# Kernel tuning notes

Hardware: AMD Instinct MI355X
Metric: run time of the kernel (lower is better)

Reference implementation:

```python
import jax, jax.numpy as jnp
import numpy as np
import math

E = 1024   # embed_size
H = 16     # heads arg (actual per-'head' dim due to source's reshape quirk)
G = E // H # 64 head-groups (treated as heads in the source code)
FF = 4 * E


def setup_inputs() -> dict:
    key = jax.random.key(0)
    ks = jax.random.split(key, 12)
    s = 1.0 / math.sqrt(E)
    inp = {
        'x': jax.random.normal(ks[0], (2, 1024, E), dtype=jnp.float32),
        # linear weights stored as (in, out); torch Linear computes x @ W.T + b
        'Wq': jax.random.uniform(ks[1], (E, E), jnp.float32, -s, s),
        'Wk': jax.random.uniform(ks[2], (E, E), jnp.float32, -s, s),
        'Wv': jax.random.uniform(ks[3], (E, E), jnp.float32, -s, s),
        'Wo': jax.random.uniform(ks[4], (E, E), jnp.float32, -s, s),
        'bo': jax.random.uniform(ks[5], (E,), jnp.float32, -s, s),
        'W1': jax.random.uniform(ks[6], (E, FF), jnp.float32, -s, s),
        'b1': jax.random.uniform(ks[7], (FF,), jnp.float32, -s, s),
        'W2': jax.random.uniform(ks[8], (FF, E), jnp.float32, -1.0 / math.sqrt(FF), 1.0 / math.sqrt(FF)),
        'b2': jax.random.uniform(ks[9], (E,), jnp.float32, -s, s),
        'g1': jnp.ones((E,), jnp.float32), 'be1': jnp.zeros((E,), jnp.float32),
        'g2': jnp.ones((E,), jnp.float32), 'be2': jnp.zeros((E,), jnp.float32),
    }
    return inp


def _layernorm(x, g, b, eps=1e-5):
    mu = jnp.mean(x, axis=-1, keepdims=True)
    var = jnp.mean(jnp.square(x - mu), axis=-1, keepdims=True)
    return (x - mu) * jax.lax.rsqrt(var + eps) * g + b


def reference(x, Wq, Wk, Wv, Wo, bo, W1, b1, W2, b2, g1, be1, g2, be2):
    B, S, _ = x.shape
    # QKV projections; faithful to source: split E into (G=E//H groups, H dims),
    # group axis acts as the 'head' axis, per-head dim is H, scale = sqrt(H).
    def split(t):  # [B,S,E] -> [B,G,S,H]
        return t.reshape(B, S, G, H).transpose(0, 2, 1, 3)
    q = split(x @ Wq)
    k = split(x @ Wk)
    v = split(x @ Wv)
    att = jnp.einsum('bgsh,bgth->bgst', q, k) / math.sqrt(H)
    causal = jnp.tril(jnp.ones((S, S), dtype=bool))  # mask==1 above diag -> -inf
    att = jnp.where(causal, att, -jnp.inf)
    att = jax.nn.softmax(att, axis=-1)
    y = jnp.einsum('bgst,bgth->bgsh', att, v)          # [B,G,S,H]
    y = y.transpose(0, 2, 1, 3).reshape(B, S, E)
    attn_out = y @ Wo + bo
    # dropout is identity at inference
    x = _layernorm(attn_out + x, g1, be1)
    ff = jax.nn.relu(x @ W1 + b1) @ W2 + b2
    x = _layernorm(ff + x, g2, be2)
    return x
```

## Files before the change

### kernel.cpp

```cpp
#include <hip/hip_runtime.h>
#include <hip/hip_bf16.h>
#include <math.h>


#define E_DIM 1024
#define S_LEN 1024
#define B_SZ  2
#define G_HEADS 64
#define H_DIM 16
#define FF_DIM 4096
#define M_ROWS (B_SZ * S_LEN)
#define QKV_N  (3 * E_DIM)

#define QSCALE 0.36067376022224085f

using bf16x8 = __attribute__((ext_vector_type(8))) short;
using f32x4  = __attribute__((ext_vector_type(4))) float;
using f32x16 = __attribute__((ext_vector_type(16))) float;
using ushort8 = __attribute__((ext_vector_type(8))) unsigned short;

static __device__ __forceinline__ unsigned short f2bf(float f) {
    union { float f; unsigned int u; } x; x.f = f;
    unsigned int r = x.u + 0x7fff + ((x.u >> 16) & 1);
    return (unsigned short)(r >> 16);
}
static __device__ __forceinline__ unsigned int pack2(float a, float b) {
    union { __hip_bfloat162 h; unsigned int u; } c;
    c.h = __float22bfloat162_rn(float2{a, b});
    return c.u;
}

__global__ __launch_bounds__(256) void cast_kernel(
    const float* __restrict__ X, unsigned short* __restrict__ Xb)
{
    const size_t i = ((size_t)blockIdx.x * 256 + threadIdx.x) * 8;
    float4 a = *(const float4*)(X + i);
    float4 b = *(const float4*)(X + i + 4);
    ushort8 o;
    o[0] = f2bf(a.x); o[1] = f2bf(a.y); o[2] = f2bf(a.z); o[3] = f2bf(a.w);
    o[4] = f2bf(b.x); o[5] = f2bf(b.y); o[6] = f2bf(b.z); o[7] = f2bf(b.w);
    *(ushort8*)(Xb + i) = o;
}

__global__ __launch_bounds__(256) void transpose_cast4_kernel(
    const float* __restrict__ W0, const float* __restrict__ W1_,
    const float* __restrict__ W2_, const float* __restrict__ W3_,
    unsigned short* __restrict__ Wt012, unsigned short* __restrict__ Wt3)
{
    __shared__ float tile[32][33];
    const int z = blockIdx.z;
    const float* W = (z == 0) ? W0 : (z == 1) ? W1_ : (z == 2) ? W2_ : W3_;
    unsigned short* Wo = (z < 3) ? (Wt012 + (size_t)z * E_DIM * E_DIM) : Wt3;
    const int n0 = blockIdx.x * 32, k0 = blockIdx.y * 32;
    const int t = threadIdx.x;
    const int r = t >> 3;
    const int c = (t & 7) * 4;

    float4 v = *(const float4*)(W + (size_t)(k0 + r) * E_DIM + n0 + c);
    tile[r][c] = v.x; tile[r][c + 1] = v.y; tile[r][c + 2] = v.z; tile[r][c + 3] = v.w;
    __syncthreads();

    ushort4 o;
    o.x = f2bf(tile[c + 0][r]); o.y = f2bf(tile[c + 1][r]);
    o.z = f2bf(tile[c + 2][r]); o.w = f2bf(tile[c + 3][r]);
    *(ushort4*)(Wo + (size_t)(n0 + r) * E_DIM + k0 + c) = o;
}

__global__ __launch_bounds__(256) void transpose_cast_ff_kernel(
    const float* __restrict__ W1_, const float* __restrict__ W2_,
    unsigned short* __restrict__ W1t, unsigned short* __restrict__ W2t)
{
    __shared__ float tile[32][33];
    const int z = blockIdx.z;
    const float* W = z ? W2_ : W1_;
    unsigned short* Wt = z ? W2t : W1t;
    const int N = z ? E_DIM : FF_DIM;
    const int K = z ? FF_DIM : E_DIM;
    const int n0 = (z ? blockIdx.y : blockIdx.x) * 32;
    const int k0 = (z ? blockIdx.x : blockIdx.y) * 32;
    const int t = threadIdx.x;
    const int r = t >> 3;
    const int c = (t & 7) * 4;

    float4 v = *(const float4*)(W + (size_t)(k0 + r) * N + n0 + c);
    tile[r][c] = v.x; tile[r][c + 1] = v.y; tile[r][c + 2] = v.z; tile[r][c + 3] = v.w;
    __syncthreads();

    ushort4 o;
    o.x = f2bf(tile[c + 0][r]); o.y = f2bf(tile[c + 1][r]);
    o.z = f2bf(tile[c + 2][r]); o.w = f2bf(tile[c + 3][r]);
    *(ushort4*)(Wt + (size_t)(n0 + r) * K + k0 + c) = o;
}

template<int ACT, int OUTBF, int SCALEQ>
__global__ __launch_bounds__(256) void gemm_mfma(
    const unsigned short* __restrict__ A,
    const unsigned short* __restrict__ Bt,
    const float* __restrict__ bias,
    float* __restrict__ C0, float* __restrict__ C1,
    unsigned short* __restrict__ Cb,
    int Krow, int Kchunk, int ldc)
{
    __shared__ __align__(16) unsigned short lds[2][12288];

    const int tid  = threadIdx.x;
    const int wave = tid >> 6;
    const int lane = tid & 63;
    const int wr = wave >> 1;
    const int wc = wave & 1;
    const int row0 = blockIdx.y * 128;
    const int col0 = blockIdx.x * 64;
    const int kbase = blockIdx.z * Kchunk;

    const int lr = lane & 15;
    const int lk = (lane >> 4) * 8;

    const int srow = (lane >> 2);
    const int scol = (lane & 3) * 8;

    f32x4 acc[4][2] = {};

    auto STAGE1 = [&](unsigned short* dstA, unsigned short* dstB, int k0) {
        #pragma unroll
        for (int i = 0; i < 2; ++i) {
            const int ci = wave + i * 4;
            const unsigned short* src =
                A + (size_t)(row0 + ci * 16 + srow) * Krow + k0 + scol;
            __builtin_amdgcn_global_load_lds(
                (const __attribute__((address_space(1))) void*)src,
                (__attribute__((address_space(3))) void*)(dstA + ci * 512),
                16, 0, 0);
        }
        {
            const unsigned short* src =
                Bt + (size_t)(col0 + wave * 16 + srow) * Krow + k0 + scol;
            __builtin_amdgcn_global_load_lds(
                (const __attribute__((address_space(1))) void*)src,
                (__attribute__((address_space(3))) void*)(dstB + wave * 512),
                16, 0, 0);
        }
    };
    auto STAGE = [&](int buf, int k0) {
        STAGE1(&lds[buf][0],    &lds[buf][4096],  k0);
        STAGE1(&lds[buf][6144], &lds[buf][10240], k0 + 32);
    };
    auto COMPUTE = [&](int buf, int sub) {
        const unsigned short* As = &lds[buf][sub * 6144];
        const unsigned short* Bs = As + 4096;
        bf16x8 a[4], b[2];
        #pragma unroll
        for (int mi = 0; mi < 4; ++mi)
            a[mi] = *(const bf16x8*)(As + (wr * 64 + mi * 16 + lr) * 32 + lk);
        #pragma unroll
        for (int ni = 0; ni < 2; ++ni)
            b[ni] = *(const bf16x8*)(Bs + (wc * 32 + ni * 16 + lr) * 32 + lk);
        #pragma unroll
        for (int mi = 0; mi < 4; ++mi)
            #pragma unroll
            for (int ni = 0; ni < 2; ++ni)
                acc[mi][ni] = __builtin_amdgcn_mfma_f32_16x16x32_bf16(
                    a[mi], b[ni], acc[mi][ni], 0, 0, 0);
    };

    const int nt = Kchunk >> 6;

    STAGE(0, kbase);
    asm volatile("s_waitcnt vmcnt(0)" ::: "memory");
    __builtin_amdgcn_s_barrier();

    int cur = 0;
    for (int t = 0; t < nt; ++t) {
        if (t + 1 < nt) STAGE(cur ^ 1, kbase + (t + 1) * 64);
        COMPUTE(cur, 0);
        COMPUTE(cur, 1);
        asm volatile("s_waitcnt vmcnt(0)" ::: "memory");
        __builtin_amdgcn_s_barrier();
        cur ^= 1;
    }

    float* Cw = blockIdx.z ? C1 : C0;
    #pragma unroll
    for (int mi = 0; mi < 4; ++mi) {
        #pragma unroll
        for (int ni = 0; ni < 2; ++ni) {
            const int cc  = col0 + wc * 32 + ni * 16 + (lane & 15);
            const int rr0 = row0 + wr * 64 + mi * 16 + ((lane >> 4) << 2);
            const float bv = bias ? bias[cc] : 0.f;
            #pragma unroll
            for (int j = 0; j < 4; ++j) {
                float v = acc[mi][ni][j] + bv;
                if (ACT == 1) v = fmaxf(v, 0.f);
                if (SCALEQ && cc < E_DIM) v *= QSCALE;
                if (OUTBF) Cb[(size_t)(rr0 + j) * ldc + cc] = f2bf(v);
                else       Cw[(size_t)(rr0 + j) * ldc + cc] = v;
            }
        }
    }
}

__global__ __launch_bounds__(256) void attn_kernel(
    const unsigned short* __restrict__ qkv, unsigned short* __restrict__ Yb)
{
    __shared__ __align__(16) unsigned short Ks[2][64 * 16];
    __shared__ __align__(16) unsigned short Vs[2][64 * 16];

    const int bi = blockIdx.x >> 7;
    const int bg = blockIdx.x & 127;
    const int g  = bg & (G_HEADS - 1);
    const int b  = bg >> 6;
    const int tid  = threadIdx.x;
    const int lane = tid & 63;
    const int l31  = lane & 31;
    const int hi   = lane >> 5;
    const int wv   = tid >> 6;
    const int tokb = b * S_LEN;

    const int cblk = 28 - 4 * bi;
    const int q0   = (cblk + wv) * 32;
    const int qrow = q0 + l31;
    const int nt64 = (cblk + 4) >> 1;

    const bf16x8 qf = *(const bf16x8*)(
        qkv + (size_t)(tokb + qrow) * QKV_N + g * H_DIM + hi * 8);

    f32x16 acc = {};
    const f32x16 fz = {};

    const int kv  = tid >> 7;
    const int h64 = (tid >> 6) & 1;
    const int skey  = h64 * 32 + (lane >> 1);
    const int shalf = lane & 1;
    const size_t sgo = (size_t)(g * H_DIM + (1 + kv) * E_DIM + shalf * 8);
    unsigned short* const sdst = (kv ? &Vs[0][0] : &Ks[0][0]) + h64 * 512;

    auto STAGE = [&](int buf, int t64) {
        const unsigned short* src =
            qkv + (size_t)(tokb + t64 * 64 + skey) * QKV_N + sgo;
        __builtin_amdgcn_global_load_lds(
            (const __attribute__((address_space(1))) void*)src,
            (__attribute__((address_space(3))) void*)(sdst + buf * 1024),
            16, 0, 0);
    };

    auto PROCESS = [&](int cur, int sub, int t0) {
        const bf16x8 kf = *(const bf16x8*)(&Ks[cur][(sub * 32 + l31) * 16 + hi * 8]);
        __builtin_amdgcn_s_setprio(1);
        f32x16 s = __builtin_amdgcn_mfma_f32_32x32x16_bf16(kf, qf, fz, 0, 0, 0);
        __builtin_amdgcn_s_setprio(0);

        float pq[16];
        if (t0 == q0) {
            #pragma unroll
            for (int r = 0; r < 16; ++r) {
                const int key = t0 + (r & 3) + 8 * (r >> 2) + 4 * hi;
                pq[r] = (key > qrow) ? 0.f : exp2f(s[r]);
            }
        } else {
            #pragma unroll
            for (int r = 0; r < 16; ++r) pq[r] = exp2f(s[r]);
        }

        unsigned int cw[8], ow[8];
        #pragma unroll
        for (int r2 = 0; r2 < 8; ++r2) cw[r2] = pack2(pq[2 * r2], pq[2 * r2 + 1]);
        #pragma unroll
        for (int r2 = 0; r2 < 8; ++r2)
            ow[r2] = (unsigned int)__shfl_xor((int)cw[r2], 32);

        const bool lo = (hi == 0);
        union { uint4 u; bf16x8 v; } pf0, pf1;
        pf0.u.x = lo ? cw[0] : ow[2];
        pf0.u.y = lo ? cw[1] : ow[3];
        pf0.u.z = lo ? ow[0] : cw[2];
        pf0.u.w = lo ? ow[1] : cw[3];
        pf1.u.x = lo ? cw[4] : ow[6];
        pf1.u.y = lo ? cw[5] : ow[7];
        pf1.u.z = lo ? ow[4] : cw[6];
        pf1.u.w = lo ? ow[5] : cw[7];

        const int hcol = l31 & 15;
        const bool isl = (l31 == 16);
        union { unsigned short s2[8]; bf16x8 v; } vb0, vb1;
        #pragma unroll
        for (int e = 0; e < 8; ++e) {
            const int kr = sub * 32 + hi * 8 + e;
            vb0.s2[e] = isl ? (unsigned short)0x3F80 : Vs[cur][kr * 16 + hcol];
            vb1.s2[e] = isl ? (unsigned short)0x3F80 : Vs[cur][(kr + 16) * 16 + hcol];
        }
        __builtin_amdgcn_s_setprio(1);
        acc = __builtin_amdgcn_mfma_f32_32x32x16_bf16(pf0.v, vb0.v, acc, 0, 0, 0);
        acc = __builtin_amdgcn_mfma_f32_32x32x16_bf16(pf1.v, vb1.v, acc, 0, 0, 0);
        __builtin_amdgcn_s_setprio(0);
    };

    STAGE(0, 0);
    asm volatile("s_waitcnt vmcnt(0)" ::: "memory");
    __builtin_amdgcn_s_barrier();

    int cur = 0;
    for (int t = 0; t < nt64; ++t) {
        if (t + 1 < nt64) STAGE(cur ^ 1, t + 1);
        #pragma unroll
        for (int sub = 0; sub < 2; ++sub) {
            const int t0 = t * 64 + sub * 32;
            if (t0 <= q0) PROCESS(cur, sub, t0);
        }
        asm volatile("s_waitcnt vmcnt(0)" ::: "memory");
        __builtin_amdgcn_s_barrier();
        cur ^= 1;
    }

    float linv[16];
    #pragma unroll
    for (int r = 0; r < 16; ++r) {
        const float lr_ = __shfl(acc[r], (hi << 5) + 16);
        linv[r] = __builtin_amdgcn_rcpf(lr_);
    }
    if (l31 < H_DIM) {
        #pragma unroll
        for (int r = 0; r < 16; ++r) {
            const int q = (r & 3) + 8 * (r >> 2) + 4 * hi;
            Yb[(size_t)(tokb + q0 + q) * E_DIM + g * H_DIM + l31] =
                f2bf(acc[r] * linv[r]);
        }
    }
}

__global__ __launch_bounds__(256) void add_ln2_kernel(
    const float* __restrict__ P0, const float* __restrict__ P1,
    const float* __restrict__ bias, const float* __restrict__ resid,
    const float* __restrict__ g, const float* __restrict__ be,
    float* __restrict__ O, unsigned short* __restrict__ Ob)
{
    const int row = blockIdx.x;
    const size_t base = (size_t)row * E_DIM;
    const int tid = threadIdx.x;

    float v[4];
    float s = 0.f;
    #pragma unroll
    for (int i = 0; i < 4; ++i) {
        int c = tid + i * 256;
        v[i] = P0[base + c] + P1[base + c] + bias[c] + resid[base + c];
        s += v[i];
    }

    __shared__ float red[256];
    red[tid] = s; __syncthreads();
    for (int st = 128; st >= 1; st >>= 1) {
        if (tid < st) red[tid] += red[tid + st];
        __syncthreads();
    }
    const float mu = red[0] * (1.f / E_DIM);
    __syncthreads();

    float s2 = 0.f;
    #pragma unroll
    for (int i = 0; i < 4; ++i) { float d = v[i] - mu; s2 += d * d; }
    red[tid] = s2; __syncthreads();
    for (int st = 128; st >= 1; st >>= 1) {
        if (tid < st) red[tid] += red[tid + st];
        __syncthreads();
    }
    const float rs = rsqrtf(red[0] * (1.f / E_DIM) + 1e-5f);

    #pragma unroll
    for (int i = 0; i < 4; ++i) {
        int c = tid + i * 256;
        float o = (v[i] - mu) * rs * g[c] + be[c];
        O[base + c] = o;
        if (Ob) Ob[base + c] = f2bf(o);
    }
}

extern "C" void kernel_launch(void* const* d_in, const int* in_sizes, int n_in,
                              void* d_out, int out_size, void* d_ws, size_t ws_size,
                              hipStream_t stream)
{
    const float* x  = (const float*)d_in[0];
    const float* Wq = (const float*)d_in[1];
    const float* Wk = (const float*)d_in[2];
    const float* Wv = (const float*)d_in[3];
    const float* Wo = (const float*)d_in[4];
    const float* bo = (const float*)d_in[5];
    const float* W1 = (const float*)d_in[6];
    const float* b1 = (const float*)d_in[7];
    const float* W2 = (const float*)d_in[8];
    const float* b2 = (const float*)d_in[9];
    const float* g1  = (const float*)d_in[10];
    const float* be1 = (const float*)d_in[11];
    const float* g2  = (const float*)d_in[12];
    const float* be2 = (const float*)d_in[13];

    char* W = (char*)d_ws;
    const size_t MB = 1024 * 1024;
    unsigned short* xb   = (unsigned short*)(W + 0 * MB);
    unsigned short* Wqkt = (unsigned short*)(W + 4 * MB);
    unsigned short* qkvb = (unsigned short*)(W + 10 * MB);
    unsigned short* yb   = (unsigned short*)(W + 22 * MB);
    unsigned short* Wot  = (unsigned short*)(W + 26 * MB);
    float* P_o0          = (float*)(W + 4 * MB);
    float* P_o1          = (float*)(W + 12 * MB);
    unsigned short* x1b  = (unsigned short*)(W + 20 * MB);
    float* x1            = (float*)(W + 28 * MB);
    unsigned short* W1t  = (unsigned short*)(W + 36 * MB);
    unsigned short* W2t  = (unsigned short*)(W + 44 * MB);
    unsigned short* ff1b = (unsigned short*)(W + 0 * MB);
    float* P_f1          = (float*)(W + 16 * MB);
    float* out           = (float*)d_out;

    dim3 blk(256);

    cast_kernel<<<dim3((M_ROWS * E_DIM) / (256 * 8)), blk, 0, stream>>>(x, xb);
    transpose_cast4_kernel<<<dim3(32, 32, 4), blk, 0, stream>>>(Wq, Wk, Wv, Wo, Wqkt, Wot);
    transpose_cast_ff_kernel<<<dim3(128, 32, 2), blk, 0, stream>>>(W1, W2, W1t, W2t);
    gemm_mfma<0, 1, 1><<<dim3(QKV_N / 64, M_ROWS / 128, 1), blk, 0, stream>>>(
        xb, Wqkt, nullptr, nullptr, nullptr, qkvb, E_DIM, E_DIM, QKV_N);
    attn_kernel<<<dim3(B_SZ * G_HEADS * 8), blk, 0, stream>>>(qkvb, yb);
    gemm_mfma<0, 0, 0><<<dim3(E_DIM / 64, M_ROWS / 128, 2), blk, 0, stream>>>(
        yb, Wot, nullptr, P_o0, P_o1, nullptr, E_DIM, E_DIM / 2, E_DIM);
    add_ln2_kernel<<<dim3(M_ROWS), blk, 0, stream>>>(P_o0, P_o1, bo, x, g1, be1, x1, x1b);
    gemm_mfma<1, 1, 0><<<dim3(FF_DIM / 64, M_ROWS / 128, 1), blk, 0, stream>>>(
        x1b, W1t, b1, nullptr, nullptr, ff1b, E_DIM, E_DIM, FF_DIM);
    gemm_mfma<0, 0, 0><<<dim3(E_DIM / 64, M_ROWS / 128, 2), blk, 0, stream>>>(
        ff1b, W2t, nullptr, out, P_f1, nullptr, FF_DIM, FF_DIM / 2, E_DIM);
    add_ln2_kernel<<<dim3(M_ROWS), blk, 0, stream>>>(out, P_f1, b2, x1, g2, be2, out, nullptr);
}
```

Measured before the change: 170.6 us.

## Stage V transposed in LDS and use permlane32 swap for P fragments

V tiles are now loaded into registers and written transposed (with a padded stride and a constant ones row for the softmax denominator) into LDS, so each lane fetches its B operand with two 16-byte vector reads instead of sixteen scalar LDS reads with per-element selects. The cross-half exchange of the P fragment uses v_permlane32_swap instead of eight shfl_xor plus selects. This trades the asynchronous global-to-LDS copy for V for a register load plus scattered scalar LDS stores per tile, and adds an lgkmcnt wait before the barrier.

```diff
diff --git a/kernel.cpp b/kernel.cpp
--- a/kernel.cpp
+++ b/kernel.cpp
@@ -13,6 +13,9 @@
 #define QKV_N  (3 * E_DIM)
 
 #define QSCALE 0.36067376022224085f
+
+#define VT_STRIDE 72
+#define VT_BUF    1224
 
 using bf16x8 = __attribute__((ext_vector_type(8))) short;
 using f32x4  = __attribute__((ext_vector_type(4))) float;
@@ -201,8 +204,8 @@
 __global__ __launch_bounds__(256) void attn_kernel(
     const unsigned short* __restrict__ qkv, unsigned short* __restrict__ Yb)
 {
-    __shared__ __align__(16) unsigned short Ks[2][64 * 16];
-    __shared__ __align__(16) unsigned short Vs[2][64 * 16];
+    __shared__ __align__(16) unsigned short Ks[2][1024];
+    __shared__ __align__(16) unsigned short Vt[2][VT_BUF];
 
     const int bi = blockIdx.x >> 7;
     const int bg = blockIdx.x & 127;
@@ -231,16 +234,28 @@
     const int skey  = h64 * 32 + (lane >> 1);
     const int shalf = lane & 1;
     const size_t sgo = (size_t)(g * H_DIM + (1 + kv) * E_DIM + shalf * 8);
-    unsigned short* const sdst = (kv ? &Vs[0][0] : &Ks[0][0]) + h64 * 512;
-
-    auto STAGE = [&](int buf, int t64) {
+
+    auto STAGE = [&](int buf, int t64, ushort8& vreg) {
         const unsigned short* src =
             qkv + (size_t)(tokb + t64 * 64 + skey) * QKV_N + sgo;
-        __builtin_amdgcn_global_load_lds(
-            (const __attribute__((address_space(1))) void*)src,
-            (__attribute__((address_space(3))) void*)(sdst + buf * 1024),
-            16, 0, 0);
-    };
+        if (kv == 0) {
+            __builtin_amdgcn_global_load_lds(
+                (const __attribute__((address_space(1))) void*)src,
+                (__attribute__((address_space(3))) void*)(&Ks[buf][h64 * 512]),
+                16, 0, 0);
+        } else {
+            vreg = *(const ushort8*)src;
+        }
+    };
+    auto WRITE_V = [&](int buf, const ushort8& vreg) {
+        if (kv == 1) {
+            #pragma unroll
+            for (int j = 0; j < 8; ++j)
+                Vt[buf][(shalf * 8 + j) * VT_STRIDE + skey] = vreg[j];
+        }
+    };
+
+    const int vrow = (l31 == 16) ? 16 : (l31 & 15);
 
     auto PROCESS = [&](int cur, int sub, int t0) {
         const bf16x8 kf = *(const bf16x8*)(&Ks[cur][(sub * 32 + l31) * 16 + hi * 8]);
@@ -260,52 +275,64 @@
             for (int r = 0; r < 16; ++r) pq[r] = exp2f(s[r]);
         }
 
-        unsigned int cw[8], ow[8];
+        unsigned int cw[8];
         #pragma unroll
         for (int r2 = 0; r2 < 8; ++r2) cw[r2] = pack2(pq[2 * r2], pq[2 * r2 + 1]);
-        #pragma unroll
-        for (int r2 = 0; r2 < 8; ++r2)
-            ow[r2] = (unsigned int)__shfl_xor((int)cw[r2], 32);
-
-        const bool lo = (hi == 0);
+
         union { uint4 u; bf16x8 v; } pf0, pf1;
-        pf0.u.x = lo ? cw[0] : ow[2];
-        pf0.u.y = lo ? cw[1] : ow[3];
-        pf0.u.z = lo ? ow[0] : cw[2];
-        pf0.u.w = lo ? ow[1] : cw[3];
-        pf1.u.x = lo ? cw[4] : ow[6];
-        pf1.u.y = lo ? cw[5] : ow[7];
-        pf1.u.z = lo ? ow[4] : cw[6];
-        pf1.u.w = lo ? ow[5] : cw[7];
-
-        const int hcol = l31 & 15;
-        const bool isl = (l31 == 16);
-        union { unsigned short s2[8]; bf16x8 v; } vb0, vb1;
-        #pragma unroll
-        for (int e = 0; e < 8; ++e) {
-            const int kr = sub * 32 + hi * 8 + e;
-            vb0.s2[e] = isl ? (unsigned short)0x3F80 : Vs[cur][kr * 16 + hcol];
-            vb1.s2[e] = isl ? (unsigned short)0x3F80 : Vs[cur][(kr + 16) * 16 + hcol];
-        }
+        {
+            unsigned int a = cw[0], c = cw[2];
+            asm volatile("v_permlane32_swap_b32 %0, %1" : "+v"(a), "+v"(c));
+            pf0.u.x = a; pf0.u.z = c;
+        }
+        {
+            unsigned int a = cw[1], c = cw[3];
+            asm volatile("v_permlane32_swap_b32 %0, %1" : "+v"(a), "+v"(c));
+            pf0.u.y = a; pf0.u.w = c;
+        }
+        {
+            unsigned int a = cw[4], c = cw[6];
+            asm volatile("v_permlane32_swap_b32 %0, %1" : "+v"(a), "+v"(c));
+            pf1.u.x = a; pf1.u.z = c;
+        }
+        {
+            unsigned int a = cw[5], c = cw[7];
+            asm volatile("v_permlane32_swap_b32 %0, %1" : "+v"(a), "+v"(c));
+            pf1.u.y = a; pf1.u.w = c;
+        }
+
+        const unsigned short* vbase =
+            &Vt[cur][vrow * VT_STRIDE + sub * 32 + hi * 8];
+        const bf16x8 vb0 = *(const bf16x8*)(vbase);
+        const bf16x8 vb1 = *(const bf16x8*)(vbase + 16);
+
         __builtin_amdgcn_s_setprio(1);
-        acc = __builtin_amdgcn_mfma_f32_32x32x16_bf16(pf0.v, vb0.v, acc, 0, 0, 0);
-        acc = __builtin_amdgcn_mfma_f32_32x32x16_bf16(pf1.v, vb1.v, acc, 0, 0, 0);
+        acc = __builtin_amdgcn_mfma_f32_32x32x16_bf16(pf0.v, vb0, acc, 0, 0, 0);
+        acc = __builtin_amdgcn_mfma_f32_32x32x16_bf16(pf1.v, vb1, acc, 0, 0, 0);
         __builtin_amdgcn_s_setprio(0);
     };
 
-    STAGE(0, 0);
-    asm volatile("s_waitcnt vmcnt(0)" ::: "memory");
-    __builtin_amdgcn_s_barrier();
+    ushort8 vreg = {};
+    STAGE(0, 0, vreg);
+    if (kv == 1) {
+        const int vt = tid - 128;
+        Vt[vt >> 6][16 * VT_STRIDE + (vt & 63)] = 0x3F80;
+    }
+    WRITE_V(0, vreg);
+    __syncthreads();
 
     int cur = 0;
     for (int t = 0; t < nt64; ++t) {
-        if (t + 1 < nt64) STAGE(cur ^ 1, t + 1);
+        ushort8 vnext = {};
+        const bool more = (t + 1 < nt64);
+        if (more) STAGE(cur ^ 1, t + 1, vnext);
         #pragma unroll
         for (int sub = 0; sub < 2; ++sub) {
             const int t0 = t * 64 + sub * 32;
             if (t0 <= q0) PROCESS(cur, sub, t0);
         }
-        asm volatile("s_waitcnt vmcnt(0)" ::: "memory");
+        if (more) WRITE_V(cur ^ 1, vnext);
+        asm volatile("s_waitcnt vmcnt(0) lgkmcnt(0)" ::: "memory");
         __builtin_amdgcn_s_barrier();
         cur ^= 1;
     }
```

Result: faster. 162.7 us (-4.7%).
